# Kernel tuning notes

Hardware: AMD Instinct MI355X
Metric: run time of the kernel (lower is better)

Reference implementation:

```python
import jax, jax.numpy as jnp
import numpy as np

N_NODES = 50000
N_EDGES = 800000
IN_FEATS = 128
N_HIDDEN = 128
N_CLASSES = 47
LN_EPS = 1e-5


def _sage_conv(h, src, dst, w_self, w_neigh, b):
    # DGL SAGEConv 'mean': out = h_dst @ W_self + mean_neigh(h_src) @ W_neigh + b
    msg = h[src]  # [E, d] gather
    agg = jax.ops.segment_sum(msg, dst, num_segments=N_NODES)
    deg = jax.ops.segment_sum(jnp.ones((src.shape[0],), h.dtype), dst, num_segments=N_NODES)
    h_neigh = agg / jnp.maximum(deg, 1.0)[:, None]  # zero-degree nodes -> 0
    return h @ w_self + h_neigh @ w_neigh + b


def _layer_norm(h, gamma, beta):
    mu = jnp.mean(h, axis=-1, keepdims=True)
    var = jnp.mean(jnp.square(h - mu), axis=-1, keepdims=True)
    return (h - mu) * jax.lax.rsqrt(var + LN_EPS) * gamma + beta


def setup_inputs() -> dict:
    key = jax.random.key(0)
    ks = jax.random.split(key, 12)
    s = 0.05
    inp = {
        "x": jax.random.normal(ks[0], (N_NODES, IN_FEATS), jnp.float32),
        "src": jax.random.randint(ks[1], (N_EDGES,), 0, N_NODES, jnp.int32),
        "dst": jax.random.randint(ks[2], (N_EDGES,), 0, N_NODES, jnp.int32),
        # layer 0
        "w_self0": jax.random.normal(ks[3], (IN_FEATS, N_HIDDEN), jnp.float32) * s,
        "w_neigh0": jax.random.normal(ks[4], (IN_FEATS, N_HIDDEN), jnp.float32) * s,
        "b0": jnp.zeros((N_HIDDEN,), jnp.float32),
        "g0": jnp.ones((N_HIDDEN,), jnp.float32),
        "be0": jnp.zeros((N_HIDDEN,), jnp.float32),
        # layer 1
        "w_self1": jax.random.normal(ks[5], (N_HIDDEN, N_HIDDEN), jnp.float32) * s,
        "w_neigh1": jax.random.normal(ks[6], (N_HIDDEN, N_HIDDEN), jnp.float32) * s,
        "b1": jnp.zeros((N_HIDDEN,), jnp.float32),
        "g1": jnp.ones((N_HIDDEN,), jnp.float32),
        "be1": jnp.zeros((N_HIDDEN,), jnp.float32),
        # layer 2 (output)
        "w_self2": jax.random.normal(ks[7], (N_HIDDEN, N_CLASSES), jnp.float32) * s,
        "w_neigh2": jax.random.normal(ks[8], (N_HIDDEN, N_CLASSES), jnp.float32) * s,
        "b2": jnp.zeros((N_CLASSES,), jnp.float32),
    }
    return inp


def reference(x, src, dst,
              w_self0, w_neigh0, b0, g0, be0,
              w_self1, w_neigh1, b1, g1, be1,
              w_self2, w_neigh2, b2):
    h = _sage_conv(x, src, dst, w_self0, w_neigh0, b0)
    h = jax.nn.relu(_layer_norm(h, g0, be0))
    h = _sage_conv(h, src, dst, w_self1, w_neigh1, b1)
    h = jax.nn.relu(_layer_norm(h, g1, be1))
    h = _sage_conv(h, src, dst, w_self2, w_neigh2, b2)
    return h
```

## Files before the change

kernel.cpp:

```cpp
#include <hip/hip_runtime.h>

#define NN 50000
#define NE 800000
#define D 128
#define NCLS 47
#define ZPAD 64
#define LN_EPS 1e-5f

__global__ void k_count(const int* __restrict__ dst, int* __restrict__ counts) {
  int i = blockIdx.x * blockDim.x + threadIdx.x;
  if (i < NE) atomicAdd(&counts[dst[i]], 1);
}

__global__ void k_scan1(const int* __restrict__ counts, int* __restrict__ excl,
                        int* __restrict__ bsum) {
  __shared__ int tmp[256];
  int t = threadIdx.x, i = blockIdx.x * 256 + t;
  int v = (i < NN) ? counts[i] : 0;
  tmp[t] = v;
  __syncthreads();
  for (int off = 1; off < 256; off <<= 1) {
    int u = (t >= off) ? tmp[t - off] : 0;
    __syncthreads();
    tmp[t] += u;
    __syncthreads();
  }
  if (i < NN) excl[i] = tmp[t] - v;
  if (t == 255) bsum[blockIdx.x] = tmp[255];
}

__global__ void k_scan2(int* __restrict__ bsum, int nb) {
  __shared__ int tmp[256];
  int t = threadIdx.x;
  int v = (t < nb) ? bsum[t] : 0;
  tmp[t] = v;
  __syncthreads();
  for (int off = 1; off < 256; off <<= 1) {
    int u = (t >= off) ? tmp[t - off] : 0;
    __syncthreads();
    tmp[t] += u;
    __syncthreads();
  }
  if (t < nb) bsum[t] = tmp[t] - v;
}

__global__ void k_scan3(int* __restrict__ indptr, const int* __restrict__ bsum,
                        int* __restrict__ cursor) {
  int i = blockIdx.x * 256 + threadIdx.x;
  if (i < NN) {
    int v = indptr[i] + bsum[i >> 8];
    indptr[i] = v;
    cursor[i] = v;
  }
  if (i == 0) indptr[NN] = NE;
}

__global__ void k_scatter(const int* __restrict__ src, const int* __restrict__ dst,
                          int* __restrict__ cursor, int* __restrict__ esrc) {
  int i = blockIdx.x * blockDim.x + threadIdx.x;
  if (i < NE) {
    int d = dst[i];
    int pos = atomicAdd(&cursor[d], 1);
    esrc[pos] = src[i];
  }
}

__global__ __launch_bounds__(256) void k_agg(const float* __restrict__ feat,
                                             const int* __restrict__ indptr,
                                             const int* __restrict__ esrc,
                                             float* __restrict__ out) {
  int w = (blockIdx.x * 256 + threadIdx.x) >> 6;
  int lane = threadIdx.x & 63;
  if (w >= NN) return;
  int beg = indptr[w], end = indptr[w + 1];
  float a0 = 0.f, a1 = 0.f;
  int e = beg;
  for (; e + 7 < end; e += 8) {
    int s0 = esrc[e],     s1 = esrc[e + 1], s2 = esrc[e + 2], s3 = esrc[e + 3];
    int s4 = esrc[e + 4], s5 = esrc[e + 5], s6 = esrc[e + 6], s7 = esrc[e + 7];
    float2 v0 = *(const float2*)(feat + (size_t)s0 * D + lane * 2);
    float2 v1 = *(const float2*)(feat + (size_t)s1 * D + lane * 2);
    float2 v2 = *(const float2*)(feat + (size_t)s2 * D + lane * 2);
    float2 v3 = *(const float2*)(feat + (size_t)s3 * D + lane * 2);
    float2 v4 = *(const float2*)(feat + (size_t)s4 * D + lane * 2);
    float2 v5 = *(const float2*)(feat + (size_t)s5 * D + lane * 2);
    float2 v6 = *(const float2*)(feat + (size_t)s6 * D + lane * 2);
    float2 v7 = *(const float2*)(feat + (size_t)s7 * D + lane * 2);
    a0 += v0.x + v1.x + v2.x + v3.x + v4.x + v5.x + v6.x + v7.x;
    a1 += v0.y + v1.y + v2.y + v3.y + v4.y + v5.y + v6.y + v7.y;
  }
  for (; e + 1 < end; e += 2) {
    int s0 = esrc[e], s1 = esrc[e + 1];
    float2 v0 = *(const float2*)(feat + (size_t)s0 * D + lane * 2);
    float2 v1 = *(const float2*)(feat + (size_t)s1 * D + lane * 2);
    a0 += v0.x + v1.x;
    a1 += v0.y + v1.y;
  }
  if (e < end) {
    float2 v0 = *(const float2*)(feat + (size_t)esrc[e] * D + lane * 2);
    a0 += v0.x;
    a1 += v0.y;
  }
  float inv = 1.0f / fmaxf((float)(end - beg), 1.0f);
  float2 o;
  o.x = a0 * inv;
  o.y = a1 * inv;
  *(float2*)(out + (size_t)w * D + lane * 2) = o;
}

__global__ __launch_bounds__(256, 5) void k_gemm_ln(
    const float* __restrict__ h, const float* __restrict__ hn,
    const float* __restrict__ ws, const float* __restrict__ wn,
    const float* __restrict__ b, const float* __restrict__ g,
    const float* __restrict__ be, float* __restrict__ out) {
  __shared__ float lds[32][256];
  int tid = threadIdx.x;
  int row0 = blockIdx.x * 32;
  for (int i = tid; i < 32 * 64; i += 256) {
    int r = i >> 6, q = i & 63;
    int row = row0 + r;
    float4 v = make_float4(0.f, 0.f, 0.f, 0.f);
    if (row < NN) {
      const float* p = (q < 32) ? (h + (size_t)row * D + q * 4)
                                : (hn + (size_t)row * D + (q - 32) * 4);
      v = *(const float4*)p;
    }
    *(float4*)&lds[r][q * 4] = v;
  }
  __syncthreads();

  int wv = tid >> 6, lane = tid & 63;
  int rbase = wv * 8;
  float acc0[8], acc1[8];
#pragma unroll
  for (int r = 0; r < 8; ++r) { acc0[r] = 0.f; acc1[r] = 0.f; }

  for (int k = 0; k < 128; k += 4) {
    float w00 = ws[(k + 0) * 128 + lane], w01 = ws[(k + 0) * 128 + lane + 64];
    float w10 = ws[(k + 1) * 128 + lane], w11 = ws[(k + 1) * 128 + lane + 64];
    float w20 = ws[(k + 2) * 128 + lane], w21 = ws[(k + 2) * 128 + lane + 64];
    float w30 = ws[(k + 3) * 128 + lane], w31 = ws[(k + 3) * 128 + lane + 64];
#pragma unroll
    for (int r = 0; r < 8; ++r) {
      float4 hv = *(const float4*)&lds[rbase + r][k];
      acc0[r] = fmaf(hv.x, w00, acc0[r]);
      acc1[r] = fmaf(hv.x, w01, acc1[r]);
      acc0[r] = fmaf(hv.y, w10, acc0[r]);
      acc1[r] = fmaf(hv.y, w11, acc1[r]);
      acc0[r] = fmaf(hv.z, w20, acc0[r]);
      acc1[r] = fmaf(hv.z, w21, acc1[r]);
      acc0[r] = fmaf(hv.w, w30, acc0[r]);
      acc1[r] = fmaf(hv.w, w31, acc1[r]);
    }
  }
  for (int k = 0; k < 128; k += 4) {
    float w00 = wn[(k + 0) * 128 + lane], w01 = wn[(k + 0) * 128 + lane + 64];
    float w10 = wn[(k + 1) * 128 + lane], w11 = wn[(k + 1) * 128 + lane + 64];
    float w20 = wn[(k + 2) * 128 + lane], w21 = wn[(k + 2) * 128 + lane + 64];
    float w30 = wn[(k + 3) * 128 + lane], w31 = wn[(k + 3) * 128 + lane + 64];
#pragma unroll
    for (int r = 0; r < 8; ++r) {
      float4 hv = *(const float4*)&lds[rbase + r][128 + k];
      acc0[r] = fmaf(hv.x, w00, acc0[r]);
      acc1[r] = fmaf(hv.x, w01, acc1[r]);
      acc0[r] = fmaf(hv.y, w10, acc0[r]);
      acc1[r] = fmaf(hv.y, w11, acc1[r]);
      acc0[r] = fmaf(hv.z, w20, acc0[r]);
      acc1[r] = fmaf(hv.z, w21, acc1[r]);
      acc0[r] = fmaf(hv.w, w30, acc0[r]);
      acc1[r] = fmaf(hv.w, w31, acc1[r]);
    }
  }

  float bj0 = b[lane], bj1 = b[lane + 64];
  float gj0 = g[lane], gj1 = g[lane + 64];
  float ej0 = be[lane], ej1 = be[lane + 64];
#pragma unroll
  for (int r = 0; r < 8; ++r) {
    float v0 = acc0[r] + bj0, v1 = acc1[r] + bj1;
    float s = v0 + v1, q2 = v0 * v0 + v1 * v1;
#pragma unroll
    for (int off = 1; off < 64; off <<= 1) {
      s += __shfl_xor(s, off, 64);
      q2 += __shfl_xor(q2, off, 64);
    }
    float mu = s * (1.0f / 128.0f);
    float var = q2 * (1.0f / 128.0f) - mu * mu;
    float rs = rsqrtf(var + LN_EPS);
    float o0 = fmaxf((v0 - mu) * rs * gj0 + ej0, 0.f);
    float o1 = fmaxf((v1 - mu) * rs * gj1 + ej1, 0.f);
    int row = row0 + rbase + r;
    if (row < NN) {
      out[(size_t)row * D + lane] = o0;
      out[(size_t)row * D + lane + 64] = o1;
    }
  }
}

__global__ __launch_bounds__(256) void k_gemm_proj2(
    const float* __restrict__ h, const float* __restrict__ ws,
    const float* __restrict__ wn, const float* __restrict__ b,
    float* __restrict__ s2p, float* __restrict__ z2) {
  __shared__ float lds[32][128];
  int tid = threadIdx.x;
  int row0 = blockIdx.x * 32;
  for (int i = tid; i < 32 * 32; i += 256) {
    int r = i >> 5, q = i & 31;
    int row = row0 + r;
    float4 v = make_float4(0.f, 0.f, 0.f, 0.f);
    if (row < NN) v = *(const float4*)(h + (size_t)row * D + q * 4);
    *(float4*)&lds[r][q * 4] = v;
  }
  __syncthreads();

  int wv = tid >> 6, lane = tid & 63;
  int rbase = wv * 8;
  bool act = lane < NCLS;
  float accS[8], accZ[8];
#pragma unroll
  for (int r = 0; r < 8; ++r) { accS[r] = 0.f; accZ[r] = 0.f; }

  for (int k = 0; k < 128; k += 4) {
    float ws0 = act ? ws[(k + 0) * NCLS + lane] : 0.f;
    float ws1 = act ? ws[(k + 1) * NCLS + lane] : 0.f;
    float ws2 = act ? ws[(k + 2) * NCLS + lane] : 0.f;
    float ws3 = act ? ws[(k + 3) * NCLS + lane] : 0.f;
    float wn0 = act ? wn[(k + 0) * NCLS + lane] : 0.f;
    float wn1 = act ? wn[(k + 1) * NCLS + lane] : 0.f;
    float wn2 = act ? wn[(k + 2) * NCLS + lane] : 0.f;
    float wn3 = act ? wn[(k + 3) * NCLS + lane] : 0.f;
#pragma unroll
    for (int r = 0; r < 8; ++r) {
      float4 hv = *(const float4*)&lds[rbase + r][k];
      accS[r] = fmaf(hv.x, ws0, accS[r]);
      accZ[r] = fmaf(hv.x, wn0, accZ[r]);
      accS[r] = fmaf(hv.y, ws1, accS[r]);
      accZ[r] = fmaf(hv.y, wn1, accZ[r]);
      accS[r] = fmaf(hv.z, ws2, accS[r]);
      accZ[r] = fmaf(hv.z, wn2, accZ[r]);
      accS[r] = fmaf(hv.w, ws3, accS[r]);
      accZ[r] = fmaf(hv.w, wn3, accZ[r]);
    }
  }

  float bj = act ? b[lane] : 0.f;
#pragma unroll
  for (int r = 0; r < 8; ++r) {
    int row = row0 + rbase + r;
    if (row < NN) {
      z2[(size_t)row * ZPAD + lane] = act ? accZ[r] : 0.f;
      s2p[(size_t)row * ZPAD + lane] = accS[r] + bj;
    }
  }
}

__global__ __launch_bounds__(256) void k_agg2(const float* __restrict__ z2,
                                              const float* __restrict__ s2p,
                                              const int* __restrict__ indptr,
                                              const int* __restrict__ esrc,
                                              float* __restrict__ out) {
  int w = (blockIdx.x * 256 + threadIdx.x) >> 6;
  int lane = threadIdx.x & 63;
  if (w >= NN) return;
  int beg = indptr[w], end = indptr[w + 1];
  float a = 0.f;
  int e = beg;
  for (; e + 7 < end; e += 8) {
    int s0 = esrc[e],     s1 = esrc[e + 1], s2 = esrc[e + 2], s3 = esrc[e + 3];
    int s4 = esrc[e + 4], s5 = esrc[e + 5], s6 = esrc[e + 6], s7 = esrc[e + 7];
    a += z2[(size_t)s0 * ZPAD + lane] + z2[(size_t)s1 * ZPAD + lane] +
         z2[(size_t)s2 * ZPAD + lane] + z2[(size_t)s3 * ZPAD + lane] +
         z2[(size_t)s4 * ZPAD + lane] + z2[(size_t)s5 * ZPAD + lane] +
         z2[(size_t)s6 * ZPAD + lane] + z2[(size_t)s7 * ZPAD + lane];
  }
  for (; e < end; ++e) a += z2[(size_t)esrc[e] * ZPAD + lane];
  float inv = 1.0f / fmaxf((float)(end - beg), 1.0f);
  if (lane < NCLS)
    out[(size_t)w * NCLS + lane] = s2p[(size_t)w * ZPAD + lane] + a * inv;
}

extern "C" void kernel_launch(void* const* d_in, const int* in_sizes, int n_in,
                              void* d_out, int out_size, void* d_ws, size_t ws_size,
                              hipStream_t stream) {
  (void)in_sizes; (void)n_in; (void)out_size; (void)ws_size;
  const float* x       = (const float*)d_in[0];
  const int*   src     = (const int*)d_in[1];
  const int*   dst     = (const int*)d_in[2];
  const float* w_self0 = (const float*)d_in[3];
  const float* w_nei0  = (const float*)d_in[4];
  const float* b0      = (const float*)d_in[5];
  const float* g0      = (const float*)d_in[6];
  const float* be0     = (const float*)d_in[7];
  const float* w_self1 = (const float*)d_in[8];
  const float* w_nei1  = (const float*)d_in[9];
  const float* b1      = (const float*)d_in[10];
  const float* g1      = (const float*)d_in[11];
  const float* be1     = (const float*)d_in[12];
  const float* w_self2 = (const float*)d_in[13];
  const float* w_nei2  = (const float*)d_in[14];
  const float* b2      = (const float*)d_in[15];
  float* outp = (float*)d_out;

  char* ws = (char*)d_ws;
  size_t off = 0;
  auto alloc = [&](size_t bytes) -> void* {
    off = (off + 255) & ~(size_t)255;
    void* p = ws + off;
    off += bytes;
    return p;
  };
  int*   counts = (int*)alloc(NN * sizeof(int));
  int*   indptr = (int*)alloc((NN + 1) * sizeof(int));
  int*   cursor = (int*)alloc(NN * sizeof(int));
  int*   bsum   = (int*)alloc(256 * sizeof(int));
  int*   esrc   = (int*)alloc(NE * sizeof(int));
  float* hn     = (float*)alloc((size_t)NN * D * sizeof(float));
  float* h1     = (float*)alloc((size_t)NN * D * sizeof(float));
  float* h2     = (float*)alloc((size_t)NN * D * sizeof(float));
  float* z2  = hn;
  float* s2p = h1;

  const int nbScan = (NN + 255) / 256;

  hipMemsetAsync(counts, 0, NN * sizeof(int), stream);
  k_count<<<(NE + 255) / 256, 256, 0, stream>>>(dst, counts);
  k_scan1<<<nbScan, 256, 0, stream>>>(counts, indptr, bsum);
  k_scan2<<<1, 256, 0, stream>>>(bsum, nbScan);
  k_scan3<<<nbScan, 256, 0, stream>>>(indptr, bsum, cursor);
  k_scatter<<<(NE + 255) / 256, 256, 0, stream>>>(src, dst, cursor, esrc);

  const int aggBlocks  = (NN * 64) / 256;
  const int gemmBlocks = (NN + 31) / 32;

  k_agg<<<aggBlocks, 256, 0, stream>>>(x, indptr, esrc, hn);
  k_gemm_ln<<<gemmBlocks, 256, 0, stream>>>(x, hn, w_self0, w_nei0, b0, g0, be0, h1);
  k_agg<<<aggBlocks, 256, 0, stream>>>(h1, indptr, esrc, hn);
  k_gemm_ln<<<gemmBlocks, 256, 0, stream>>>(h1, hn, w_self1, w_nei1, b1, g1, be1, h2);
  k_gemm_proj2<<<gemmBlocks, 256, 0, stream>>>(h2, w_self2, w_nei2, b2, s2p, z2);
  k_agg2<<<aggBlocks, 256, 0, stream>>>(z2, s2p, indptr, esrc, outp);
}
```

Before: 530.0 us.

## Split wavefront into half-waves for wider gathers and prefetch GEMM weights

```diff
diff --git a/kernel.cpp b/kernel.cpp
--- a/kernel.cpp
+++ b/kernel.cpp
@@ -72,43 +72,40 @@
   int w = (blockIdx.x * 256 + threadIdx.x) >> 6;
   int lane = threadIdx.x & 63;
   if (w >= NN) return;
+  int l32 = lane & 31;
+  int col = l32 * 4;
   int beg = indptr[w], end = indptr[w + 1];
-  float a0 = 0.f, a1 = 0.f;
-  int e = beg;
-  for (; e + 7 < end; e += 8) {
-    int s0 = esrc[e],     s1 = esrc[e + 1], s2 = esrc[e + 2], s3 = esrc[e + 3];
-    int s4 = esrc[e + 4], s5 = esrc[e + 5], s6 = esrc[e + 6], s7 = esrc[e + 7];
-    float2 v0 = *(const float2*)(feat + (size_t)s0 * D + lane * 2);
-    float2 v1 = *(const float2*)(feat + (size_t)s1 * D + lane * 2);
-    float2 v2 = *(const float2*)(feat + (size_t)s2 * D + lane * 2);
-    float2 v3 = *(const float2*)(feat + (size_t)s3 * D + lane * 2);
-    float2 v4 = *(const float2*)(feat + (size_t)s4 * D + lane * 2);
-    float2 v5 = *(const float2*)(feat + (size_t)s5 * D + lane * 2);
-    float2 v6 = *(const float2*)(feat + (size_t)s6 * D + lane * 2);
-    float2 v7 = *(const float2*)(feat + (size_t)s7 * D + lane * 2);
-    a0 += v0.x + v1.x + v2.x + v3.x + v4.x + v5.x + v6.x + v7.x;
-    a1 += v0.y + v1.y + v2.y + v3.y + v4.y + v5.y + v6.y + v7.y;
-  }
-  for (; e + 1 < end; e += 2) {
-    int s0 = esrc[e], s1 = esrc[e + 1];
-    float2 v0 = *(const float2*)(feat + (size_t)s0 * D + lane * 2);
-    float2 v1 = *(const float2*)(feat + (size_t)s1 * D + lane * 2);
-    a0 += v0.x + v1.x;
-    a1 += v0.y + v1.y;
-  }
-  if (e < end) {
-    float2 v0 = *(const float2*)(feat + (size_t)esrc[e] * D + lane * 2);
-    a0 += v0.x;
-    a1 += v0.y;
-  }
-  float inv = 1.0f / fmaxf((float)(end - beg), 1.0f);
-  float2 o;
-  o.x = a0 * inv;
-  o.y = a1 * inv;
-  *(float2*)(out + (size_t)w * D + lane * 2) = o;
-}
-
-__global__ __launch_bounds__(256, 5) void k_gemm_ln(
+  float4 a = make_float4(0.f, 0.f, 0.f, 0.f);
+  int e = beg + (lane >> 5);
+  for (; e + 14 < end; e += 16) {
+    int idx[8];
+#pragma unroll
+    for (int j = 0; j < 8; ++j) idx[j] = esrc[e + 2 * j];
+    float4 v[8];
+#pragma unroll
+    for (int j = 0; j < 8; ++j)
+      v[j] = *(const float4*)(feat + (size_t)idx[j] * D + col);
+#pragma unroll
+    for (int j = 0; j < 8; ++j) {
+      a.x += v[j].x; a.y += v[j].y; a.z += v[j].z; a.w += v[j].w;
+    }
+  }
+  for (; e < end; e += 2) {
+    float4 v = *(const float4*)(feat + (size_t)esrc[e] * D + col);
+    a.x += v.x; a.y += v.y; a.z += v.z; a.w += v.w;
+  }
+  a.x += __shfl_xor(a.x, 32, 64);
+  a.y += __shfl_xor(a.y, 32, 64);
+  a.z += __shfl_xor(a.z, 32, 64);
+  a.w += __shfl_xor(a.w, 32, 64);
+  if (lane < 32) {
+    float inv = 1.0f / fmaxf((float)(end - beg), 1.0f);
+    float4 o = make_float4(a.x * inv, a.y * inv, a.z * inv, a.w * inv);
+    *(float4*)(out + (size_t)w * D + col) = o;
+  }
+}
+
+__global__ __launch_bounds__(256, 4) void k_gemm_ln(
     const float* __restrict__ h, const float* __restrict__ hn,
     const float* __restrict__ ws, const float* __restrict__ wn,
     const float* __restrict__ b, const float* __restrict__ g,
@@ -135,41 +132,36 @@
 #pragma unroll
   for (int r = 0; r < 8; ++r) { acc0[r] = 0.f; acc1[r] = 0.f; }
 
-  for (int k = 0; k < 128; k += 4) {
-    float w00 = ws[(k + 0) * 128 + lane], w01 = ws[(k + 0) * 128 + lane + 64];
-    float w10 = ws[(k + 1) * 128 + lane], w11 = ws[(k + 1) * 128 + lane + 64];
-    float w20 = ws[(k + 2) * 128 + lane], w21 = ws[(k + 2) * 128 + lane + 64];
-    float w30 = ws[(k + 3) * 128 + lane], w31 = ws[(k + 3) * 128 + lane + 64];
+  float cw[8], nw[8];
+#pragma unroll
+  for (int j = 0; j < 4; ++j) {
+    cw[2 * j]     = ws[j * 128 + lane];
+    cw[2 * j + 1] = ws[j * 128 + lane + 64];
+  }
+#pragma unroll 2
+  for (int c = 0; c < 64; ++c) {
+    int cn = (c + 1 < 64) ? c + 1 : 63;
+    const float* np = ((cn & 32) ? wn : ws) + (cn & 31) * 512;
+#pragma unroll
+    for (int j = 0; j < 4; ++j) {
+      nw[2 * j]     = np[j * 128 + lane];
+      nw[2 * j + 1] = np[j * 128 + lane + 64];
+    }
+    int kc = c * 4;
 #pragma unroll
     for (int r = 0; r < 8; ++r) {
-      float4 hv = *(const float4*)&lds[rbase + r][k];
-      acc0[r] = fmaf(hv.x, w00, acc0[r]);
-      acc1[r] = fmaf(hv.x, w01, acc1[r]);
-      acc0[r] = fmaf(hv.y, w10, acc0[r]);
-      acc1[r] = fmaf(hv.y, w11, acc1[r]);
-      acc0[r] = fmaf(hv.z, w20, acc0[r]);
-      acc1[r] = fmaf(hv.z, w21, acc1[r]);
-      acc0[r] = fmaf(hv.w, w30, acc0[r]);
-      acc1[r] = fmaf(hv.w, w31, acc1[r]);
-    }
-  }
-  for (int k = 0; k < 128; k += 4) {
-    float w00 = wn[(k + 0) * 128 + lane], w01 = wn[(k + 0) * 128 + lane + 64];
-    float w10 = wn[(k + 1) * 128 + lane], w11 = wn[(k + 1) * 128 + lane + 64];
-    float w20 = wn[(k + 2) * 128 + lane], w21 = wn[(k + 2) * 128 + lane + 64];
-    float w30 = wn[(k + 3) * 128 + lane], w31 = wn[(k + 3) * 128 + lane + 64];
-#pragma unroll
-    for (int r = 0; r < 8; ++r) {
-      float4 hv = *(const float4*)&lds[rbase + r][128 + k];
-      acc0[r] = fmaf(hv.x, w00, acc0[r]);
-      acc1[r] = fmaf(hv.x, w01, acc1[r]);
-      acc0[r] = fmaf(hv.y, w10, acc0[r]);
-      acc1[r] = fmaf(hv.y, w11, acc1[r]);
-      acc0[r] = fmaf(hv.z, w20, acc0[r]);
-      acc1[r] = fmaf(hv.z, w21, acc1[r]);
-      acc0[r] = fmaf(hv.w, w30, acc0[r]);
-      acc1[r] = fmaf(hv.w, w31, acc1[r]);
-    }
+      float4 hv = *(const float4*)&lds[rbase + r][kc];
+      acc0[r] = fmaf(hv.x, cw[0], acc0[r]);
+      acc1[r] = fmaf(hv.x, cw[1], acc1[r]);
+      acc0[r] = fmaf(hv.y, cw[2], acc0[r]);
+      acc1[r] = fmaf(hv.y, cw[3], acc1[r]);
+      acc0[r] = fmaf(hv.z, cw[4], acc0[r]);
+      acc1[r] = fmaf(hv.z, cw[5], acc1[r]);
+      acc0[r] = fmaf(hv.w, cw[6], acc0[r]);
+      acc1[r] = fmaf(hv.w, cw[7], acc1[r]);
+    }
+#pragma unroll
+    for (int j = 0; j < 8; ++j) cw[j] = nw[j];
   }
 
   float bj0 = b[lane], bj1 = b[lane + 64];
@@ -197,7 +189,7 @@
   }
 }
 
-__global__ __launch_bounds__(256) void k_gemm_proj2(
+__global__ __launch_bounds__(256, 4) void k_gemm_proj2(
     const float* __restrict__ h, const float* __restrict__ ws,
     const float* __restrict__ wn, const float* __restrict__ b,
     float* __restrict__ s2p, float* __restrict__ z2) {
@@ -220,27 +212,35 @@
 #pragma unroll
   for (int r = 0; r < 8; ++r) { accS[r] = 0.f; accZ[r] = 0.f; }
 
-  for (int k = 0; k < 128; k += 4) {
-    float ws0 = act ? ws[(k + 0) * NCLS + lane] : 0.f;
-    float ws1 = act ? ws[(k + 1) * NCLS + lane] : 0.f;
-    float ws2 = act ? ws[(k + 2) * NCLS + lane] : 0.f;
-    float ws3 = act ? ws[(k + 3) * NCLS + lane] : 0.f;
-    float wn0 = act ? wn[(k + 0) * NCLS + lane] : 0.f;
-    float wn1 = act ? wn[(k + 1) * NCLS + lane] : 0.f;
-    float wn2 = act ? wn[(k + 2) * NCLS + lane] : 0.f;
-    float wn3 = act ? wn[(k + 3) * NCLS + lane] : 0.f;
+  float cw[8], nw[8];
+#pragma unroll
+  for (int j = 0; j < 4; ++j) {
+    cw[j]     = act ? ws[j * NCLS + lane] : 0.f;
+    cw[4 + j] = act ? wn[j * NCLS + lane] : 0.f;
+  }
+#pragma unroll 2
+  for (int c = 0; c < 32; ++c) {
+    int cn = (c + 1 < 32) ? c + 1 : 31;
+#pragma unroll
+    for (int j = 0; j < 4; ++j) {
+      nw[j]     = act ? ws[(cn * 4 + j) * NCLS + lane] : 0.f;
+      nw[4 + j] = act ? wn[(cn * 4 + j) * NCLS + lane] : 0.f;
+    }
+    int kc = c * 4;
 #pragma unroll
     for (int r = 0; r < 8; ++r) {
-      float4 hv = *(const float4*)&lds[rbase + r][k];
-      accS[r] = fmaf(hv.x, ws0, accS[r]);
-      accZ[r] = fmaf(hv.x, wn0, accZ[r]);
-      accS[r] = fmaf(hv.y, ws1, accS[r]);
-      accZ[r] = fmaf(hv.y, wn1, accZ[r]);
-      accS[r] = fmaf(hv.z, ws2, accS[r]);
-      accZ[r] = fmaf(hv.z, wn2, accZ[r]);
-      accS[r] = fmaf(hv.w, ws3, accS[r]);
-      accZ[r] = fmaf(hv.w, wn3, accZ[r]);
-    }
+      float4 hv = *(const float4*)&lds[rbase + r][kc];
+      accS[r] = fmaf(hv.x, cw[0], accS[r]);
+      accZ[r] = fmaf(hv.x, cw[4], accZ[r]);
+      accS[r] = fmaf(hv.y, cw[1], accS[r]);
+      accZ[r] = fmaf(hv.y, cw[5], accZ[r]);
+      accS[r] = fmaf(hv.z, cw[2], accS[r]);
+      accZ[r] = fmaf(hv.z, cw[6], accZ[r]);
+      accS[r] = fmaf(hv.w, cw[3], accS[r]);
+      accZ[r] = fmaf(hv.w, cw[7], accZ[r]);
+    }
+#pragma unroll
+    for (int j = 0; j < 8; ++j) cw[j] = nw[j];
   }
 
   float bj = act ? b[lane] : 0.f;
@@ -262,21 +262,36 @@
   int w = (blockIdx.x * 256 + threadIdx.x) >> 6;
   int lane = threadIdx.x & 63;
   if (w >= NN) return;
+  int l32 = lane & 31;
+  int col = l32 * 2;
   int beg = indptr[w], end = indptr[w + 1];
-  float a = 0.f;
-  int e = beg;
-  for (; e + 7 < end; e += 8) {
-    int s0 = esrc[e],     s1 = esrc[e + 1], s2 = esrc[e + 2], s3 = esrc[e + 3];
-    int s4 = esrc[e + 4], s5 = esrc[e + 5], s6 = esrc[e + 6], s7 = esrc[e + 7];
-    a += z2[(size_t)s0 * ZPAD + lane] + z2[(size_t)s1 * ZPAD + lane] +
-         z2[(size_t)s2 * ZPAD + lane] + z2[(size_t)s3 * ZPAD + lane] +
-         z2[(size_t)s4 * ZPAD + lane] + z2[(size_t)s5 * ZPAD + lane] +
-         z2[(size_t)s6 * ZPAD + lane] + z2[(size_t)s7 * ZPAD + lane];
-  }
-  for (; e < end; ++e) a += z2[(size_t)esrc[e] * ZPAD + lane];
-  float inv = 1.0f / fmaxf((float)(end - beg), 1.0f);
-  if (lane < NCLS)
-    out[(size_t)w * NCLS + lane] = s2p[(size_t)w * ZPAD + lane] + a * inv;
+  float ax = 0.f, ay = 0.f;
+  int e = beg + (lane >> 5);
+  for (; e + 14 < end; e += 16) {
+    int idx[8];
+#pragma unroll
+    for (int j = 0; j < 8; ++j) idx[j] = esrc[e + 2 * j];
+    float2 v[8];
+#pragma unroll
+    for (int j = 0; j < 8; ++j)
+      v[j] = *(const float2*)(z2 + (size_t)idx[j] * ZPAD + col);
+#pragma unroll
+    for (int j = 0; j < 8; ++j) { ax += v[j].x; ay += v[j].y; }
+  }
+  for (; e < end; e += 2) {
+    float2 v = *(const float2*)(z2 + (size_t)esrc[e] * ZPAD + col);
+    ax += v.x;
+    ay += v.y;
+  }
+  ax += __shfl_xor(ax, 32, 64);
+  ay += __shfl_xor(ay, 32, 64);
+  if (lane < 32) {
+    float inv = 1.0f / fmaxf((float)(end - beg), 1.0f);
+    if (col < NCLS)
+      out[(size_t)w * NCLS + col] = s2p[(size_t)w * ZPAD + col] + ax * inv;
+    if (col + 1 < NCLS)
+      out[(size_t)w * NCLS + col + 1] = s2p[(size_t)w * ZPAD + col + 1] + ay * inv;
+  }
 }
 
 extern "C" void kernel_launch(void* const* d_in, const int* in_sizes, int n_in,
```

Measured after the change: 543.6 us. +2.6%, slower.
